# Kernel tuning notes

Hardware: AMD Instinct MI355X
Metric: run time of the kernel (lower is better)

## Reference

```python
import jax, jax.numpy as jnp
import numpy as np

B, N, D, H = 4, 2048, 1024, 16
DH = D // H


def setup_inputs() -> dict:
    key = jax.random.key(0)
    ks = jax.random.split(key, 9)
    s = 1.0 / np.sqrt(D)
    return {
        "x": jax.random.normal(ks[0], (B, N, D), dtype=jnp.float32),
        "Wq": jax.random.normal(ks[1], (D, D), dtype=jnp.float32) * s,
        "bq": jax.random.normal(ks[2], (D,), dtype=jnp.float32) * 0.01,
        "Wk": jax.random.normal(ks[3], (D, D), dtype=jnp.float32) * s,
        "bk": jax.random.normal(ks[4], (D,), dtype=jnp.float32) * 0.01,
        "Wv": jax.random.normal(ks[5], (D, D), dtype=jnp.float32) * s,
        "bv": jax.random.normal(ks[6], (D,), dtype=jnp.float32) * 0.01,
        "Wp": jax.random.normal(ks[7], (D, D), dtype=jnp.float32) * s,
        "bp": jax.random.normal(ks[8], (D,), dtype=jnp.float32) * 0.01,
    }


def reference(x, Wq, bq, Wk, bk, Wv, bv, Wp, bp):
    b, n, d = x.shape
    # torch Linear: x @ W.T + b; reshape to (b, h, n, dh)
    def heads(W, bias):
        y = jnp.einsum('bnd,ed->bne', x, W) + bias
        return y.reshape(b, n, H, DH).transpose(0, 2, 1, 3)
    q, k, v = heads(Wq, bq), heads(Wk, bk), heads(Wv, bv)
    # NOTE: source multiplies by sqrt(d_head) (bug in original), kept faithfully
    scale = jnp.sqrt(jnp.float32(DH))
    att = jnp.einsum('bhqd,bhkd->bhqk', q, k) * scale
    causal = jnp.triu(jnp.ones((n, n), dtype=bool), k=1)  # True above diagonal
    att = jnp.where(causal, -jnp.inf, att)
    att = jax.nn.softmax(att, axis=-1)
    # dropout is eval-mode identity
    out = jnp.einsum('bhqk,bhkd->bhqd', att, v)
    out = out.transpose(0, 2, 1, 3).reshape(b, n, d)
    return jnp.einsum('bnd,ed->bne', out, Wp) + bp
```

## Files before the change

kernel.cpp:

```cpp
#include <hip/hip_runtime.h>
#include <hip/hip_fp16.h>


typedef _Float16 half8 __attribute__((ext_vector_type(8)));
typedef _Float16 half4 __attribute__((ext_vector_type(4)));
typedef float f32x4 __attribute__((ext_vector_type(4)));
typedef unsigned int u32x4 __attribute__((ext_vector_type(4)));

#define DEV __device__ __forceinline__
#define MFMA16(a, b, c) __builtin_amdgcn_mfma_f32_16x16x32_f16(a, b, c, 0, 0, 0)

DEV void gload_lds16(const void* g, void* l) {
  __builtin_amdgcn_global_load_lds(
      (const __attribute__((address_space(1))) void*)g,
      (__attribute__((address_space(3))) void*)l, 16, 0, 0);
}

__global__ __launch_bounds__(256) void cast_all(
    const float* __restrict__ x, const float* __restrict__ Wq,
    const float* __restrict__ Wk, const float* __restrict__ Wv,
    const float* __restrict__ Wp, __half* __restrict__ xb,
    __half* __restrict__ wqkv, __half* __restrict__ wpb) {
  int i = blockIdx.x * 256 + threadIdx.x;
  const float* s;
  __half* d;
  int j;
  if (i < 1048576) {
    s = x; d = xb; j = i;
  } else {
    int k = i - 1048576;
    int sel = k >> 17;
    j = k & 131071;
    s = (sel == 0) ? Wq : (sel == 1) ? Wk : (sel == 2) ? Wv : Wp;
    d = (sel == 3) ? wpb : (wqkv + sel * 1048576);
  }
  const float4* sp = (const float4*)s + (size_t)j * 2;
  float4 a = sp[0], b = sp[1];
  half8 h;
  h[0] = (_Float16)a.x; h[1] = (_Float16)a.y; h[2] = (_Float16)a.z; h[3] = (_Float16)a.w;
  h[4] = (_Float16)b.x; h[5] = (_Float16)b.y; h[6] = (_Float16)b.z; h[7] = (_Float16)b.w;
  *((half8*)d + j) = h;
}

template <int MODE>
__global__ __launch_bounds__(256) void gemm128(
    const __half* __restrict__ A, const __half* __restrict__ Bm,
    const float* __restrict__ b0, const float* __restrict__ b1,
    const float* __restrict__ b2, __half* __restrict__ oh,
    __half* __restrict__ vtp, float* __restrict__ of) {
  const int m0 = blockIdx.y * 128;
  const int n0 = blockIdx.x * 128;
  const int tid = threadIdx.x;
  const int w = tid >> 6, lane = tid & 63;
  const int lr = lane & 15, lq = lane >> 4;
  const int wr = w >> 1, wc = w & 1;

  __shared__ alignas(16) __half As[128 * 64];
  __shared__ alignas(16) __half Bs[128 * 64];

  f32x4 acc[4][4] = {};

  const int arow = lane >> 3;
  const int acol = (lane & 7) * 8;
  const __half* Agp = A + ((size_t)m0 + w * 32 + arow) * 1024 + acol;
  const __half* Bgp = Bm + ((size_t)n0 + w * 32 + arow) * 1024 + acol;

  for (int kt = 0; kt < 16; ++kt) {
#pragma unroll
    for (int j = 0; j < 4; ++j) {
      gload_lds16(Agp + j * 8192 + kt * 64, As + (w * 4 + j) * 512);
      gload_lds16(Bgp + j * 8192 + kt * 64, Bs + (w * 4 + j) * 512);
    }
    __syncthreads();
#pragma unroll
    for (int s = 0; s < 2; ++s) {
      half8 af[4], bf[4];
#pragma unroll
      for (int i = 0; i < 4; ++i) {
        af[i] = *(const half8*)(As + (wr * 64 + i * 16 + lr) * 64 + s * 32 + lq * 8);
        bf[i] = *(const half8*)(Bs + (wc * 64 + i * 16 + lr) * 64 + s * 32 + lq * 8);
      }
#pragma unroll
      for (int mi = 0; mi < 4; ++mi)
#pragma unroll
        for (int ni = 0; ni < 4; ++ni)
          acc[mi][ni] = MFMA16(af[mi], bf[ni], acc[mi][ni]);
    }
    __syncthreads();
  }

  if (MODE == 0) {
#pragma unroll
    for (int ni = 0; ni < 4; ++ni) {
      int col = n0 + wc * 64 + ni * 16 + lr;
      int t = col >> 10, e = col & 1023;
      const float* bb = (t == 0) ? b0 : ((t == 1) ? b1 : b2);
      float bias = bb[e];
      int hh = e >> 6, dh = e & 63;
      if (t == 2) {
#pragma unroll
        for (int mi = 0; mi < 4; ++mi) {
          int row = m0 + wr * 64 + mi * 16 + lq * 4;
          int b_ = row >> 11, n = row & 2047;
          half4 h;
#pragma unroll
          for (int r = 0; r < 4; ++r) h[r] = (_Float16)(acc[mi][ni][r] + bias);
          *(half4*)(vtp + (size_t)(b_ * 16 + hh) * 131072 + (size_t)dh * 2048 + n) = h;
        }
      } else {
        float scale = (t == 0) ? 11.541560327111707f : 1.0f;
        __half* base = oh + (size_t)t * 8388608 + dh;
#pragma unroll
        for (int mi = 0; mi < 4; ++mi)
#pragma unroll
          for (int r = 0; r < 4; ++r) {
            int row = m0 + wr * 64 + mi * 16 + lq * 4 + r;
            int b_ = row >> 11, n = row & 2047;
            float v = (acc[mi][ni][r] + bias) * scale;
            base[(((size_t)(b_ * 16 + hh) * 2048 + n) * 64)] = __float2half(v);
          }
      }
    }
  } else {
#pragma unroll
    for (int ni = 0; ni < 4; ++ni) {
      int col = n0 + wc * 64 + ni * 16 + lr;
      float bias = b0[col];
#pragma unroll
      for (int mi = 0; mi < 4; ++mi)
#pragma unroll
        for (int r = 0; r < 4; ++r) {
          int row = m0 + wr * 64 + mi * 16 + lq * 4 + r;
          of[(size_t)row * 1024 + col] = acc[mi][ni][r] + bias;
        }
    }
  }
}

__global__ __launch_bounds__(512, 4) void attn128(const __half* __restrict__ Q,
                                                  const __half* __restrict__ K,
                                                  const __half* __restrict__ Vt,
                                                  __half* __restrict__ O) {
  const int wg = blockIdx.x;
  const int bh = wg & 63;
  const int qt = 15 - (wg >> 6);
  const int b = bh >> 4, h = bh & 15;
  const int tid = threadIdx.x;
  const int w = tid >> 6, lane = tid & 63;
  const int lr = lane & 15, lq = lane >> 4;
  const int hi = lane >> 5;
  const int sA = (lane & 15) | ((lane & 16) << 1);
  const int sB = sA + 16;

  __shared__ alignas(16) __half Ks[2][4096];
  __shared__ alignas(16) __half Vs[2][4096];

  const __half* Kb = K + (size_t)bh * 131072;
  const __half* Vb = Vt + (size_t)bh * 131072;

  const int srow = lane >> 3;
  const int scol = ((lane & 7) ^ srow) * 8;

  const int q0 = qt * 128;
  const int ktend = 2 * qt + 2;
  const int rmin = q0 + w * 16;
  const int myq = rmin + lr;

  const __half* Qp = Q + ((size_t)bh * 2048 + q0 + w * 16) * 64;
  half8 qf0 = *(const half8*)(Qp + lr * 64 + lq * 8);
  half8 qf1 = *(const half8*)(Qp + lr * 64 + 32 + lq * 8);

  f32x4 oacc[4] = {};
  float m = -INFINITY, l = 0.f;

  gload_lds16(Kb + (size_t)(0 + w * 8 + srow) * 64 + scol, Ks[0] + w * 512);
  gload_lds16(Vb + (size_t)(w * 8 + srow) * 2048 + 0 + scol, Vs[0] + w * 512);
  asm volatile("" ::: "memory");

  for (int kt = 0; kt < ktend; ++kt) {
    const int cur = kt & 1;
    const int k0 = kt * 64;
    if (kt + 1 < ktend) {
      const int kn = k0 + 64;
      gload_lds16(Kb + (size_t)(kn + w * 8 + srow) * 64 + scol,
                  Ks[cur ^ 1] + w * 512);
      gload_lds16(Vb + (size_t)(w * 8 + srow) * 2048 + kn + scol,
                  Vs[cur ^ 1] + w * 512);
      asm volatile("s_waitcnt vmcnt(2)" ::: "memory");
    } else {
      asm volatile("s_waitcnt vmcnt(0)" ::: "memory");
    }
    __builtin_amdgcn_s_barrier();
    asm volatile("" ::: "memory");

    const char* Kc = (const char*)Ks[cur];
    const char* Vc = (const char*)Vs[cur];
    const bool active = (k0 <= rmin + 15);
    if (active) {
      f32x4 sacc[4] = {};
      __builtin_amdgcn_s_setprio(1);
#pragma unroll
      for (int nt = 0; nt < 4; ++nt) {
        int row = nt * 16 + lr;
        half8 kb0 = *(const half8*)(Kc + ((row * 128 + lq * 16) ^ ((row & 7) << 4)));
        half8 kb1 = *(const half8*)(Kc + ((row * 128 + 64 + lq * 16) ^ ((row & 7) << 4)));
        sacc[nt] = MFMA16(kb0, qf0, sacc[nt]);
        sacc[nt] = MFMA16(kb1, qf1, sacc[nt]);
      }
      __builtin_amdgcn_s_setprio(0);

      if (k0 + 63 > rmin) {
#pragma unroll
        for (int nt = 0; nt < 4; ++nt)
#pragma unroll
          for (int r = 0; r < 4; ++r) {
            int key = k0 + nt * 16 + lq * 4 + r;
            if (key > myq) sacc[nt][r] = -INFINITY;
          }
      }

      float rm = fmaxf(fmaxf(fmaxf(sacc[0][0], sacc[0][1]),
                             fmaxf(sacc[0][2], sacc[0][3])),
                       fmaxf(fmaxf(sacc[1][0], sacc[1][1]),
                             fmaxf(sacc[1][2], sacc[1][3])));
      rm = fmaxf(rm, fmaxf(fmaxf(fmaxf(sacc[2][0], sacc[2][1]),
                                 fmaxf(sacc[2][2], sacc[2][3])),
                           fmaxf(fmaxf(sacc[3][0], sacc[3][1]),
                                 fmaxf(sacc[3][2], sacc[3][3]))));
      rm = fmaxf(rm, __shfl_xor(rm, 16));
      rm = fmaxf(rm, __shfl_xor(rm, 32));

      if (__any(rm > m + 8.f)) {
        float mn = fmaxf(m, rm);
        float al = __builtin_amdgcn_exp2f(m - mn);
        m = mn;
        l *= al;
        float al4[4];
#pragma unroll
        for (int r = 0; r < 4; ++r) al4[r] = __shfl(al, lq * 4 + r);
#pragma unroll
        for (int dt = 0; dt < 4; ++dt)
#pragma unroll
          for (int r = 0; r < 4; ++r) oacc[dt][r] *= al4[r];
      }

      float ps = 0.f;
#pragma unroll
      for (int nt = 0; nt < 4; ++nt) {
        float p0 = __builtin_amdgcn_exp2f(sacc[nt][0] - m);
        float p1 = __builtin_amdgcn_exp2f(sacc[nt][1] - m);
        float p2 = __builtin_amdgcn_exp2f(sacc[nt][2] - m);
        float p3 = __builtin_amdgcn_exp2f(sacc[nt][3] - m);
        sacc[nt][0] = p0; sacc[nt][1] = p1;
        sacc[nt][2] = p2; sacc[nt][3] = p3;
        ps += (p0 + p1) + (p2 + p3);
      }
      ps += __shfl_xor(ps, 16);
      ps += __shfl_xor(ps, 32);
      l += ps;

      unsigned ph[8];
#pragma unroll
      for (int nt = 0; nt < 4; ++nt) {
        __half2 a = __floats2half2_rn(sacc[nt][0], sacc[nt][1]);
        __half2 bq_ = __floats2half2_rn(sacc[nt][2], sacc[nt][3]);
        ph[2 * nt] = *(unsigned*)&a;
        ph[2 * nt + 1] = *(unsigned*)&bq_;
      }

      u32x4 fa, fb;
      {
        unsigned t0, t1;
        t0 = __shfl((int)ph[0], sA); t1 = __shfl((int)ph[2], sA);
        fa[0] = hi ? t1 : t0;
        t0 = __shfl((int)ph[1], sA); t1 = __shfl((int)ph[3], sA);
        fa[1] = hi ? t1 : t0;
        t0 = __shfl((int)ph[0], sB); t1 = __shfl((int)ph[2], sB);
        fa[2] = hi ? t1 : t0;
        t0 = __shfl((int)ph[1], sB); t1 = __shfl((int)ph[3], sB);
        fa[3] = hi ? t1 : t0;
        t0 = __shfl((int)ph[4], sA); t1 = __shfl((int)ph[6], sA);
        fb[0] = hi ? t1 : t0;
        t0 = __shfl((int)ph[5], sA); t1 = __shfl((int)ph[7], sA);
        fb[1] = hi ? t1 : t0;
        t0 = __shfl((int)ph[4], sB); t1 = __shfl((int)ph[6], sB);
        fb[2] = hi ? t1 : t0;
        t0 = __shfl((int)ph[5], sB); t1 = __shfl((int)ph[7], sB);
        fb[3] = hi ? t1 : t0;
      }
      half8 pa0 = *(half8*)&fa;
      half8 pa1 = *(half8*)&fb;

      __builtin_amdgcn_s_setprio(1);
#pragma unroll
      for (int dt = 0; dt < 4; ++dt) {
        int row = dt * 16 + lr;
        half8 vb0 = *(const half8*)(Vc + ((row * 128 + lq * 16) ^ ((row & 7) << 4)));
        half8 vb1 = *(const half8*)(Vc + ((row * 128 + 64 + lq * 16) ^ ((row & 7) << 4)));
        oacc[dt] = MFMA16(pa0, vb0, oacc[dt]);
        oacc[dt] = MFMA16(pa1, vb1, oacc[dt]);
      }
      __builtin_amdgcn_s_setprio(0);
    }
    asm volatile("s_waitcnt lgkmcnt(0)" ::: "memory");
    __builtin_amdgcn_s_barrier();
    asm volatile("" ::: "memory");
  }

  float linv = 1.0f / l;
  float inv4[4];
#pragma unroll
  for (int r = 0; r < 4; ++r) inv4[r] = __shfl(linv, lq * 4 + r);
  __half* Op = O + ((size_t)b * 2048 + q0 + w * 16) * 1024 + h * 64;
#pragma unroll
  for (int dt = 0; dt < 4; ++dt)
#pragma unroll
    for (int r = 0; r < 4; ++r)
      Op[(size_t)(lq * 4 + r) * 1024 + dt * 16 + lr] =
          __float2half(oacc[dt][r] * inv4[r]);
}

extern "C" void kernel_launch(void* const* d_in, const int* in_sizes, int n_in,
                              void* d_out, int out_size, void* d_ws,
                              size_t ws_size, hipStream_t stream) {
  const float* x = (const float*)d_in[0];
  const float* Wq = (const float*)d_in[1];
  const float* bq = (const float*)d_in[2];
  const float* Wk = (const float*)d_in[3];
  const float* bk = (const float*)d_in[4];
  const float* Wv = (const float*)d_in[5];
  const float* bv = (const float*)d_in[6];
  const float* Wp = (const float*)d_in[7];
  const float* bp = (const float*)d_in[8];

  char* ws = (char*)d_ws;
  const size_t XB = 0;
  const size_t WQKV = XB + 16777216;
  const size_t WPB = WQKV + 6291456;
  const size_t QKV = WPB + 2097152;
  const size_t VT = QKV + 50331648;
  const size_t OB = VT + 16777216;

  __half* xb = (__half*)(ws + XB);
  __half* wqkv = (__half*)(ws + WQKV);
  __half* wpb = (__half*)(ws + WPB);
  __half* qkv = (__half*)(ws + QKV);
  __half* vt = (__half*)(ws + VT);
  __half* ob = (__half*)(ws + OB);

  cast_all<<<6144, 256, 0, stream>>>(x, Wq, Wk, Wv, Wp, xb, wqkv, wpb);

  gemm128<0><<<dim3(24, 64), 256, 0, stream>>>(xb, wqkv, bq, bk, bv, qkv, vt,
                                               nullptr);
  attn128<<<dim3(1024), 512, 0, stream>>>(qkv, qkv + 8388608, vt, ob);
  gemm128<1><<<dim3(8, 64), 256, 0, stream>>>(ob, wpb, bp, nullptr, nullptr,
                                              nullptr, nullptr, (float*)d_out);
}
```

Before: 184.4 us.

## Give each attention wave two query row groups and use 256-thread blocks

The attention kernel now uses 4 waves per block, each handling 32 query rows as two 16-row groups. Every K/V fragment read from LDS now feeds twice as many MFMAs, and each thread stages two rows of the K/V tile. The query-tile order across the grid is also permuted into zig-zag groups to balance causal work between concurrently running blocks. The cost is higher register pressure from the doubled accumulators and fewer waves available to hide latency.

```diff
diff --git a/kernel.cpp b/kernel.cpp
--- a/kernel.cpp
+++ b/kernel.cpp
@@ -137,20 +137,24 @@
   }
 }
 
-__global__ __launch_bounds__(512, 4) void attn128(const __half* __restrict__ Q,
+__global__ __launch_bounds__(256, 4) void attn128(const __half* __restrict__ Q,
                                                   const __half* __restrict__ K,
                                                   const __half* __restrict__ Vt,
                                                   __half* __restrict__ O) {
   const int wg = blockIdx.x;
   const int bh = wg & 63;
-  const int qt = 15 - (wg >> 6);
+  const int a2 = wg >> 6, g4 = a2 >> 2, pos = a2 & 3;
+  const int qt = (g4 == 0) ? 15 - pos
+               : (g4 == 1) ? 8 + pos
+               : (g4 == 2) ? 7 - pos
+                           : pos;
   const int b = bh >> 4, h = bh & 15;
   const int tid = threadIdx.x;
   const int w = tid >> 6, lane = tid & 63;
   const int lr = lane & 15, lq = lane >> 4;
   const int hi = lane >> 5;
-  const int sA = (lane & 15) | ((lane & 16) << 1);
-  const int sB = sA + 16;
+  const int sAl = (lane & 15) | ((lane & 16) << 1);
+  const int sBl = sAl + 16;
 
   __shared__ alignas(16) __half Ks[2][4096];
   __shared__ alignas(16) __half Vs[2][4096];
@@ -158,35 +162,124 @@
   const __half* Kb = K + (size_t)bh * 131072;
   const __half* Vb = Vt + (size_t)bh * 131072;
 
-  const int srow = lane >> 3;
-  const int scol = ((lane & 7) ^ srow) * 8;
+  const int srow0 = tid >> 3;
+  const int srow1 = srow0 + 32;
+  const int scol = ((tid & 7) ^ (srow0 & 7)) * 8;
+
+#define STAGE(t, buf)                                                          \
+  do {                                                                         \
+    gload_lds16(Kb + (size_t)((t)*64 + srow0) * 64 + scol, Ks[buf] + tid * 8); \
+    gload_lds16(Kb + (size_t)((t)*64 + srow1) * 64 + scol,                     \
+                Ks[buf] + 2048 + tid * 8);                                     \
+    gload_lds16(Vb + (size_t)srow0 * 2048 + (t)*64 + scol, Vs[buf] + tid * 8); \
+    gload_lds16(Vb + (size_t)srow1 * 2048 + (t)*64 + scol,                     \
+                Vs[buf] + 2048 + tid * 8);                                     \
+  } while (0)
 
   const int q0 = qt * 128;
   const int ktend = 2 * qt + 2;
-  const int rmin = q0 + w * 16;
-  const int myq = rmin + lr;
-
-  const __half* Qp = Q + ((size_t)bh * 2048 + q0 + w * 16) * 64;
-  half8 qf0 = *(const half8*)(Qp + lr * 64 + lq * 8);
-  half8 qf1 = *(const half8*)(Qp + lr * 64 + 32 + lq * 8);
-
-  f32x4 oacc[4] = {};
-  float m = -INFINITY, l = 0.f;
-
-  gload_lds16(Kb + (size_t)(0 + w * 8 + srow) * 64 + scol, Ks[0] + w * 512);
-  gload_lds16(Vb + (size_t)(w * 8 + srow) * 2048 + 0 + scol, Vs[0] + w * 512);
+  const int rmin = q0 + w * 32;
+  const int myqa = rmin + lr;
+  const int myqb = rmin + 16 + lr;
+
+  const __half* Qpa = Q + ((size_t)bh * 2048 + rmin) * 64;
+  half8 qf0a = *(const half8*)(Qpa + lr * 64 + lq * 8);
+  half8 qf1a = *(const half8*)(Qpa + lr * 64 + 32 + lq * 8);
+  half8 qf0b = *(const half8*)(Qpa + (16 + lr) * 64 + lq * 8);
+  half8 qf1b = *(const half8*)(Qpa + (16 + lr) * 64 + 32 + lq * 8);
+
+  f32x4 oacca[4] = {}, oaccb[4] = {};
+  float ma = -INFINITY, la = 0.f, mb = -INFINITY, lb = 0.f;
+
+  STAGE(0, 0);
   asm volatile("" ::: "memory");
+
+  auto smgrp = [&](f32x4* sacc, float& m, float& l, int myq, int k0,
+                   bool needmask, f32x4* oacc, half8& pa0, half8& pa1) {
+    if (needmask) {
+#pragma unroll
+      for (int nt = 0; nt < 4; ++nt)
+#pragma unroll
+        for (int r = 0; r < 4; ++r) {
+          int key = k0 + nt * 16 + lq * 4 + r;
+          if (key > myq) sacc[nt][r] = -INFINITY;
+        }
+    }
+    float rm = fmaxf(fmaxf(fmaxf(sacc[0][0], sacc[0][1]),
+                           fmaxf(sacc[0][2], sacc[0][3])),
+                     fmaxf(fmaxf(sacc[1][0], sacc[1][1]),
+                           fmaxf(sacc[1][2], sacc[1][3])));
+    rm = fmaxf(rm, fmaxf(fmaxf(fmaxf(sacc[2][0], sacc[2][1]),
+                               fmaxf(sacc[2][2], sacc[2][3])),
+                         fmaxf(fmaxf(sacc[3][0], sacc[3][1]),
+                               fmaxf(sacc[3][2], sacc[3][3]))));
+    rm = fmaxf(rm, __shfl_xor(rm, 16));
+    rm = fmaxf(rm, __shfl_xor(rm, 32));
+    if (__any(rm > m + 8.f)) {
+      float mn = fmaxf(m, rm);
+      float al = __builtin_amdgcn_exp2f(m - mn);
+      m = mn;
+      l *= al;
+      float al4[4];
+#pragma unroll
+      for (int r = 0; r < 4; ++r) al4[r] = __shfl(al, lq * 4 + r);
+#pragma unroll
+      for (int dt = 0; dt < 4; ++dt)
+#pragma unroll
+        for (int r = 0; r < 4; ++r) oacc[dt][r] *= al4[r];
+    }
+    float ps = 0.f;
+#pragma unroll
+    for (int nt = 0; nt < 4; ++nt) {
+      float p0 = __builtin_amdgcn_exp2f(sacc[nt][0] - m);
+      float p1 = __builtin_amdgcn_exp2f(sacc[nt][1] - m);
+      float p2 = __builtin_amdgcn_exp2f(sacc[nt][2] - m);
+      float p3 = __builtin_amdgcn_exp2f(sacc[nt][3] - m);
+      sacc[nt][0] = p0; sacc[nt][1] = p1;
+      sacc[nt][2] = p2; sacc[nt][3] = p3;
+      ps += (p0 + p1) + (p2 + p3);
+    }
+    ps += __shfl_xor(ps, 16);
+    ps += __shfl_xor(ps, 32);
+    l += ps;
+    unsigned ph[8];
+#pragma unroll
+    for (int nt = 0; nt < 4; ++nt) {
+      __half2 pha = __floats2half2_rn(sacc[nt][0], sacc[nt][1]);
+      __half2 phb = __floats2half2_rn(sacc[nt][2], sacc[nt][3]);
+      ph[2 * nt] = *(unsigned*)&pha;
+      ph[2 * nt + 1] = *(unsigned*)&phb;
+    }
+    u32x4 fa, fb;
+    {
+      unsigned t0, t1;
+      t0 = __shfl((int)ph[0], sAl); t1 = __shfl((int)ph[2], sAl);
+      fa[0] = hi ? t1 : t0;
+      t0 = __shfl((int)ph[1], sAl); t1 = __shfl((int)ph[3], sAl);
+      fa[1] = hi ? t1 : t0;
+      t0 = __shfl((int)ph[0], sBl); t1 = __shfl((int)ph[2], sBl);
+      fa[2] = hi ? t1 : t0;
+      t0 = __shfl((int)ph[1], sBl); t1 = __shfl((int)ph[3], sBl);
+      fa[3] = hi ? t1 : t0;
+      t0 = __shfl((int)ph[4], sAl); t1 = __shfl((int)ph[6], sAl);
+      fb[0] = hi ? t1 : t0;
+      t0 = __shfl((int)ph[5], sAl); t1 = __shfl((int)ph[7], sAl);
+      fb[1] = hi ? t1 : t0;
+      t0 = __shfl((int)ph[4], sBl); t1 = __shfl((int)ph[6], sBl);
+      fb[2] = hi ? t1 : t0;
+      t0 = __shfl((int)ph[5], sBl); t1 = __shfl((int)ph[7], sBl);
+      fb[3] = hi ? t1 : t0;
+    }
+    pa0 = *(half8*)&fa;
+    pa1 = *(half8*)&fb;
+  };
 
   for (int kt = 0; kt < ktend; ++kt) {
     const int cur = kt & 1;
     const int k0 = kt * 64;
     if (kt + 1 < ktend) {
-      const int kn = k0 + 64;
-      gload_lds16(Kb + (size_t)(kn + w * 8 + srow) * 64 + scol,
-                  Ks[cur ^ 1] + w * 512);
-      gload_lds16(Vb + (size_t)(w * 8 + srow) * 2048 + kn + scol,
-                  Vs[cur ^ 1] + w * 512);
-      asm volatile("s_waitcnt vmcnt(2)" ::: "memory");
+      STAGE(kt + 1, cur ^ 1);
+      asm volatile("s_waitcnt vmcnt(4)" ::: "memory");
     } else {
       asm volatile("s_waitcnt vmcnt(0)" ::: "memory");
     }
@@ -195,101 +288,24 @@
 
     const char* Kc = (const char*)Ks[cur];
     const char* Vc = (const char*)Vs[cur];
-    const bool active = (k0 <= rmin + 15);
-    if (active) {
-      f32x4 sacc[4] = {};
+    if (k0 <= rmin + 31) {
+      f32x4 sa[4] = {}, sb[4] = {};
       __builtin_amdgcn_s_setprio(1);
 #pragma unroll
       for (int nt = 0; nt < 4; ++nt) {
         int row = nt * 16 + lr;
         half8 kb0 = *(const half8*)(Kc + ((row * 128 + lq * 16) ^ ((row & 7) << 4)));
         half8 kb1 = *(const half8*)(Kc + ((row * 128 + 64 + lq * 16) ^ ((row & 7) << 4)));
-        sacc[nt] = MFMA16(kb0, qf0, sacc[nt]);
-        sacc[nt] = MFMA16(kb1, qf1, sacc[nt]);
+        sa[nt] = MFMA16(kb0, qf0a, sa[nt]);
+        sa[nt] = MFMA16(kb1, qf1a, sa[nt]);
+        sb[nt] = MFMA16(kb0, qf0b, sb[nt]);
+        sb[nt] = MFMA16(kb1, qf1b, sb[nt]);
       }
       __builtin_amdgcn_s_setprio(0);
 
-      if (k0 + 63 > rmin) {
-#pragma unroll
-        for (int nt = 0; nt < 4; ++nt)
-#pragma unroll
-          for (int r = 0; r < 4; ++r) {
-            int key = k0 + nt * 16 + lq * 4 + r;
-            if (key > myq) sacc[nt][r] = -INFINITY;
-          }
-      }
-
-      float rm = fmaxf(fmaxf(fmaxf(sacc[0][0], sacc[0][1]),
-                             fmaxf(sacc[0][2], sacc[0][3])),
-                       fmaxf(fmaxf(sacc[1][0], sacc[1][1]),
-                             fmaxf(sacc[1][2], sacc[1][3])));
-      rm = fmaxf(rm, fmaxf(fmaxf(fmaxf(sacc[2][0], sacc[2][1]),
-                                 fmaxf(sacc[2][2], sacc[2][3])),
-                           fmaxf(fmaxf(sacc[3][0], sacc[3][1]),
-                                 fmaxf(sacc[3][2], sacc[3][3]))));
-      rm = fmaxf(rm, __shfl_xor(rm, 16));
-      rm = fmaxf(rm, __shfl_xor(rm, 32));
-
-      if (__any(rm > m + 8.f)) {
-        float mn = fmaxf(m, rm);
-        float al = __builtin_amdgcn_exp2f(m - mn);
-        m = mn;
-        l *= al;
-        float al4[4];
-#pragma unroll
-        for (int r = 0; r < 4; ++r) al4[r] = __shfl(al, lq * 4 + r);
-#pragma unroll
-        for (int dt = 0; dt < 4; ++dt)
-#pragma unroll
-          for (int r = 0; r < 4; ++r) oacc[dt][r] *= al4[r];
-      }
-
-      float ps = 0.f;
-#pragma unroll
-      for (int nt = 0; nt < 4; ++nt) {
-        float p0 = __builtin_amdgcn_exp2f(sacc[nt][0] - m);
-        float p1 = __builtin_amdgcn_exp2f(sacc[nt][1] - m);
-        float p2 = __builtin_amdgcn_exp2f(sacc[nt][2] - m);
-        float p3 = __builtin_amdgcn_exp2f(sacc[nt][3] - m);
-        sacc[nt][0] = p0; sacc[nt][1] = p1;
-        sacc[nt][2] = p2; sacc[nt][3] = p3;
-        ps += (p0 + p1) + (p2 + p3);
-      }
-      ps += __shfl_xor(ps, 16);
-      ps += __shfl_xor(ps, 32);
-      l += ps;
-
-      unsigned ph[8];
-#pragma unroll
-      for (int nt = 0; nt < 4; ++nt) {
-        __half2 a = __floats2half2_rn(sacc[nt][0], sacc[nt][1]);
-        __half2 bq_ = __floats2half2_rn(sacc[nt][2], sacc[nt][3]);
-        ph[2 * nt] = *(unsigned*)&a;
-        ph[2 * nt + 1] = *(unsigned*)&bq_;
-      }
-
-      u32x4 fa, fb;
-      {
-        unsigned t0, t1;
-        t0 = __shfl((int)ph[0], sA); t1 = __shfl((int)ph[2], sA);
-        fa[0] = hi ? t1 : t0;
-        t0 = __shfl((int)ph[1], sA); t1 = __shfl((int)ph[3], sA);
-        fa[1] = hi ? t1 : t0;
-        t0 = __shfl((int)ph[0], sB); t1 = __shfl((int)ph[2], sB);
-        fa[2] = hi ? t1 : t0;
-        t0 = __shfl((int)ph[1], sB); t1 = __shfl((int)ph[3], sB);
-        fa[3] = hi ? t1 : t0;
-        t0 = __shfl((int)ph[4], sA); t1 = __shfl((int)ph[6], sA);
-        fb[0] = hi ? t1 : t0;
-        t0 = __shfl((int)ph[5], sA); t1 = __shfl((int)ph[7], sA);
-        fb[1] = hi ? t1 : t0;
-        t0 = __shfl((int)ph[4], sB); t1 = __shfl((int)ph[6], sB);
-        fb[2] = hi ? t1 : t0;
-        t0 = __shfl((int)ph[5], sB); t1 = __shfl((int)ph[7], sB);
-        fb[3] = hi ? t1 : t0;
-      }
-      half8 pa0 = *(half8*)&fa;
-      half8 pa1 = *(half8*)&fb;
+      half8 paa0, paa1, pab0, pab1;
+      smgrp(sa, ma, la, myqa, k0, k0 + 63 > rmin, oacca, paa0, paa1);
+      smgrp(sb, mb, lb, myqb, k0, k0 + 63 > rmin + 16, oaccb, pab0, pab1);
 
       __builtin_amdgcn_s_setprio(1);
 #pragma unroll
@@ -297,8 +313,10 @@
         int row = dt * 16 + lr;
         half8 vb0 = *(const half8*)(Vc + ((row * 128 + lq * 16) ^ ((row & 7) << 4)));
         half8 vb1 = *(const half8*)(Vc + ((row * 128 + 64 + lq * 16) ^ ((row & 7) << 4)));
-        oacc[dt] = MFMA16(pa0, vb0, oacc[dt]);
-        oacc[dt] = MFMA16(pa1, vb1, oacc[dt]);
+        oacca[dt] = MFMA16(paa0, vb0, oacca[dt]);
+        oacca[dt] = MFMA16(paa1, vb1, oacca[dt]);
+        oaccb[dt] = MFMA16(pab0, vb0, oaccb[dt]);
+        oaccb[dt] = MFMA16(pab1, vb1, oaccb[dt]);
       }
       __builtin_amdgcn_s_setprio(0);
     }
@@ -307,17 +325,24 @@
     asm volatile("" ::: "memory");
   }
 
-  float linv = 1.0f / l;
-  float inv4[4];
-#pragma unroll
-  for (int r = 0; r < 4; ++r) inv4[r] = __shfl(linv, lq * 4 + r);
-  __half* Op = O + ((size_t)b * 2048 + q0 + w * 16) * 1024 + h * 64;
+  float linva = 1.0f / la, linvb = 1.0f / lb;
+  float inva[4], invb[4];
+#pragma unroll
+  for (int r = 0; r < 4; ++r) {
+    inva[r] = __shfl(linva, lq * 4 + r);
+    invb[r] = __shfl(linvb, lq * 4 + r);
+  }
+  __half* Opa = O + ((size_t)b * 2048 + rmin) * 1024 + h * 64;
 #pragma unroll
   for (int dt = 0; dt < 4; ++dt)
 #pragma unroll
-    for (int r = 0; r < 4; ++r)
-      Op[(size_t)(lq * 4 + r) * 1024 + dt * 16 + lr] =
-          __float2half(oacc[dt][r] * inv4[r]);
+    for (int r = 0; r < 4; ++r) {
+      Opa[(size_t)(lq * 4 + r) * 1024 + dt * 16 + lr] =
+          __float2half(oacca[dt][r] * inva[r]);
+      Opa[(size_t)(16 + lq * 4 + r) * 1024 + dt * 16 + lr] =
+          __float2half(oaccb[dt][r] * invb[r]);
+    }
+#undef STAGE
 }
 
 extern "C" void kernel_launch(void* const* d_in, const int* in_sizes, int n_in,
@@ -352,7 +377,7 @@
 
   gemm128<0><<<dim3(24, 64), 256, 0, stream>>>(xb, wqkv, bq, bk, bv, qkv, vt,
                                                nullptr);
-  attn128<<<dim3(1024), 512, 0, stream>>>(qkv, qkv + 8388608, vt, ob);
+  attn128<<<dim3(1024), 256, 0, stream>>>(qkv, qkv + 8388608, vt, ob);
   gemm128<1><<<dim3(8, 64), 256, 0, stream>>>(ob, wpb, bp, nullptr, nullptr,
                                               nullptr, nullptr, (float*)d_out);
 }
```

Result: slower. 190.8 us (+3.5%).
